# Kernel optimization log

Hardware: AMD Instinct MI355X
Metric: run time of the kernel (lower is better)

The kernel has to match this reference:

```python
import jax, jax.numpy as jnp
import numpy as np

TAIL_BOUND = 3.0
MIN_BIN_WIDTH = 1e-3
MIN_BIN_HEIGHT = 1e-3
SEARCH_EPS = 1e-6


def setup_inputs() -> dict:
    key = jax.random.key(0)
    k1, k2, k3, k4, k5 = jax.random.split(key, 5)
    B, D, K = 8192, 256, 8
    return {
        "x": jax.random.normal(k1, (B, D), dtype=jnp.float32),
        "w_": jax.random.normal(k2, (B, D, K), dtype=jnp.float32),
        "h_": jax.random.normal(k3, (B, D, K), dtype=jnp.float32),
        "dl_": jax.random.normal(k4, (B, D, 1), dtype=jnp.float32),
        "dr_": jax.random.normal(k5, (B, D, 1), dtype=jnp.float32),
    }


def _cumknots(unnorm, min_bin):
    # softmax -> min-width floor -> cumsum with exact 0/1 endpoints
    num_bins = unnorm.shape[-1]
    w = jax.nn.softmax(unnorm, axis=-1)
    w = min_bin + (1.0 - min_bin * num_bins) * w
    cum = jnp.cumsum(w, axis=-1)
    cum = cum.at[..., -1].set(1.0)
    pad = [(0, 0)] * (cum.ndim - 1) + [(1, 0)]
    cum = jnp.pad(cum, pad)
    return w, cum


def reference(x, w_, h_, dl_, dr_):
    num_bins = w_.shape[-1]
    left = bottom = -TAIL_BOUND
    right = top = TAIL_BOUND

    inside = (x >= left) & (x <= right)

    # map to unit interval; clamp keeps masked-out lanes numerically safe
    t = jnp.clip((x - left) / (right - left), 0.0, 1.0)

    widths, cumwidths = _cumknots(w_, MIN_BIN_WIDTH)       # [B,D,K], [B,D,K+1]
    heights, cumheights = _cumknots(h_, MIN_BIN_HEIGHT)

    slopes = heights / widths                              # [B,D,K]
    min1 = jnp.minimum(jnp.abs(slopes[..., :-1]), jnp.abs(slopes[..., 1:]))
    min2 = 0.5 * (widths[..., 1:] * slopes[..., :-1] + widths[..., :-1] * slopes[..., 1:]) \
           / (widths[..., :-1] + widths[..., 1:])
    mins = jnp.minimum(min1, min2)                         # [B,D,K-1]

    d_left = jax.nn.sigmoid(dl_) * 3.0 * slopes[..., :1]
    d_right = jax.nn.sigmoid(dr_) * 3.0 * slopes[..., -1:]
    d_mid = mins * (jnp.sign(slopes[..., :-1]) + jnp.sign(slopes[..., 1:]))
    derivs = jnp.concatenate([d_left, d_mid, d_right], axis=-1)  # [B,D,K+1]

    a = (derivs[..., :-1] + derivs[..., 1:] - 2.0 * slopes) / widths ** 2
    b = (3.0 * slopes - 2.0 * derivs[..., :-1] - derivs[..., 1:]) / widths
    c = derivs[..., :-1]
    d = cumheights[..., :-1]

    # searchsorted: sum(t >= knots) - 1, with eps bump on the last knot
    knots = cumwidths.at[..., -1].add(SEARCH_EPS)
    bin_idx = jnp.sum((t[..., None] >= knots).astype(jnp.int32), axis=-1) - 1
    bin_idx = jnp.clip(bin_idx, 0, num_bins - 1)[..., None]  # [B,D,1]

    take = lambda arr: jnp.take_along_axis(arr, bin_idx, axis=-1)[..., 0]
    ia, ib, ic, id_ = take(a), take(b), take(c), take(d)
    lw = take(cumwidths)

    sx = t - lw
    out_s = ia * sx ** 3 + ib * sx ** 2 + ic * sx + id_
    lad_s = jnp.log(jnp.abs(3.0 * ia * sx ** 2 + 2.0 * ib * sx + ic))

    out_s = jnp.clip(out_s, 0.0, 1.0) * (top - bottom) + bottom
    lad_s = lad_s + jnp.log(top - bottom) - jnp.log(right - left)

    outputs = jnp.where(inside, out_s, x)          # identity tails
    logabsdet = jnp.where(inside, lad_s, 0.0)
    return outputs, logabsdet
```

## Files before the change

### kernel.cpp

```cpp
#include <hip/hip_runtime.h>
#include <math.h>


constexpr int K = 8;
constexpr int E = 4;
constexpr float TAIL = 3.0f;
constexpr float MIN_BIN = 0.001f;
constexpr float SEARCH_EPS = 1e-6f;

typedef float vfloat4 __attribute__((ext_vector_type(4)));

__device__ __forceinline__ float rcpf(float v) {
    return __builtin_amdgcn_rcpf(v);
}

__global__ __launch_bounds__(256) void cbs_kernel(
    const float* __restrict__ x_,
    const float* __restrict__ w_,
    const float* __restrict__ h_,
    const float* __restrict__ dl_,
    const float* __restrict__ dr_,
    float* __restrict__ out,
    float* __restrict__ lad,
    int n)
{
    const int t  = blockIdx.x * blockDim.x + threadIdx.x;
    const int e0 = t * E;
    if (e0 >= n) return;

    const vfloat4* w4 = (const vfloat4*)w_ + 2 * (size_t)e0;
    const vfloat4* h4 = (const vfloat4*)h_ + 2 * (size_t)e0;
    vfloat4 wv[2 * E], hv[2 * E];
    #pragma unroll
    for (int q = 0; q < 2 * E; q++) wv[q] = w4[q];
    #pragma unroll
    for (int q = 0; q < 2 * E; q++) hv[q] = h4[q];
    vfloat4 xv4  = ((const vfloat4*)x_)[t];
    vfloat4 dl4  = ((const vfloat4*)dl_)[t];
    vfloat4 dr4  = ((const vfloat4*)dr_)[t];

    float outs[E], lads[E];

    #pragma unroll
    for (int e = 0; e < E; e++) {
        float wr[K] = {wv[2*e].x, wv[2*e].y, wv[2*e].z, wv[2*e].w,
                       wv[2*e+1].x, wv[2*e+1].y, wv[2*e+1].z, wv[2*e+1].w};
        float hr[K] = {hv[2*e].x, hv[2*e].y, hv[2*e].z, hv[2*e].w,
                       hv[2*e+1].x, hv[2*e+1].y, hv[2*e+1].z, hv[2*e+1].w};
        const float xv = xv4[e], dlv = dl4[e], drv = dr4[e];

        float sw = 0.0f;
        #pragma unroll
        for (int k = 0; k < K; k++) { wr[k] = __expf(wr[k]); sw += wr[k]; }
        float cs = (1.0f - MIN_BIN * K) * rcpf(sw);
        #pragma unroll
        for (int k = 0; k < K; k++) wr[k] = MIN_BIN + cs * wr[k];

        float sh = 0.0f;
        #pragma unroll
        for (int k = 0; k < K; k++) { hr[k] = __expf(hr[k]); sh += hr[k]; }
        float csh = (1.0f - MIN_BIN * K) * rcpf(sh);
        #pragma unroll
        for (int k = 0; k < K; k++) hr[k] = MIN_BIN + csh * hr[k];

        float cw[K + 1]; cw[0] = 0.0f;
        #pragma unroll
        for (int k = 0; k < K; k++) cw[k + 1] = cw[k] + wr[k];
        float ch[K + 1]; ch[0] = 0.0f;
        #pragma unroll
        for (int k = 0; k < K; k++) ch[k + 1] = ch[k] + hr[k];

        float s[K];
        #pragma unroll
        for (int k = 0; k < K; k++) s[k] = hr[k] * rcpf(wr[k]);

        float dv[K + 1];
        dv[0] = rcpf(1.0f + __expf(-dlv)) * 3.0f * s[0];
        dv[K] = rcpf(1.0f + __expf(-drv)) * 3.0f * s[K - 1];
        #pragma unroll
        for (int k = 0; k < K - 1; k++) {
            float two_m1 = 2.0f * fminf(s[k], s[k + 1]);
            float m2x = (wr[k + 1] * s[k] + wr[k] * s[k + 1])
                        * rcpf(wr[k] + wr[k + 1]);
            dv[k + 1] = fminf(two_m1, m2x);
        }

        float tt = (xv + TAIL) * (1.0f / (2.0f * TAIL));
        tt = fminf(fmaxf(tt, 0.0f), 1.0f);

        int bin = 0;
        #pragma unroll
        for (int jj = 1; jj < K; jj++) bin += (tt >= cw[jj]) ? 1 : 0;
        bin += (tt >= 1.0f + SEARCH_EPS) ? 1 : 0;
        if (bin > K - 1) bin = K - 1;

        float wk = wr[0], sk = s[0], d0 = dv[0], d1 = dv[1], lw = cw[0], dd = ch[0];
        #pragma unroll
        for (int k = 1; k < K; k++) {
            bool sel = (bin == k);
            wk = sel ? wr[k]     : wk;
            sk = sel ? s[k]      : sk;
            d0 = sel ? dv[k]     : d0;
            d1 = sel ? dv[k + 1] : d1;
            lw = sel ? cw[k]     : lw;
            dd = sel ? ch[k]     : dd;
        }

        float inv_wk = rcpf(wk);
        float ia = (d0 + d1 - 2.0f * sk) * inv_wk * inv_wk;
        float ib = (3.0f * sk - 2.0f * d0 - d1) * inv_wk;
        float ic = d0;

        float sx = tt - lw;
        float out_s = ((ia * sx + ib) * sx + ic) * sx + dd;
        float der   = (3.0f * ia * sx + 2.0f * ib) * sx + ic;
        float lad_s = __logf(fabsf(der));

        out_s = fminf(fmaxf(out_s, 0.0f), 1.0f) * (2.0f * TAIL) - TAIL;

        bool inside = (xv >= -TAIL) && (xv <= TAIL);
        outs[e] = inside ? out_s : xv;
        lads[e] = inside ? lad_s : 0.0f;
    }

    vfloat4 o4 = {outs[0], outs[1], outs[2], outs[3]};
    vfloat4 l4 = {lads[0], lads[1], lads[2], lads[3]};
    __builtin_nontemporal_store(o4, (vfloat4*)out + t);
    __builtin_nontemporal_store(l4, (vfloat4*)lad + t);
}

extern "C" void kernel_launch(void* const* d_in, const int* in_sizes, int n_in,
                              void* d_out, int out_size, void* d_ws, size_t ws_size,
                              hipStream_t stream) {
    const float* x  = (const float*)d_in[0];
    const float* w  = (const float*)d_in[1];
    const float* h  = (const float*)d_in[2];
    const float* dl = (const float*)d_in[3];
    const float* dr = (const float*)d_in[4];
    int n = in_sizes[0];
    float* out = (float*)d_out;
    float* lad = out + n;

    const int threads = 256;
    const int per_block = threads * E;
    const int blocks = (n + per_block - 1) / per_block;
    cbs_kernel<<<blocks, threads, 0, stream>>>(x, w, h, dl, dr, out, lad, n);
}
```

Baseline: 187.7 us.

## Use block-strided element mapping for coalesced loads and add occupancy hint

Each thread now handles elements spaced 256 apart instead of four contiguous ones. Adjacent lanes therefore read adjacent 32-byte w/h records, which aims to improve memory coalescing. All loads are issued up front behind a sched_barrier, and launch_bounds gains a min-blocks hint to limit register use. In exchange, the x/dl/dr loads and the output stores go from vector to scalar. The bounds check is also removed, so the kernel assumes n is a multiple of 1024.

```diff
diff --git a/kernel.cpp b/kernel.cpp
--- a/kernel.cpp
+++ b/kernel.cpp
@@ -14,7 +14,7 @@
     return __builtin_amdgcn_rcpf(v);
 }
 
-__global__ __launch_bounds__(256) void cbs_kernel(
+__global__ __launch_bounds__(256, 2) void cbs_kernel(
     const float* __restrict__ x_,
     const float* __restrict__ w_,
     const float* __restrict__ h_,
@@ -24,30 +24,33 @@
     float* __restrict__ lad,
     int n)
 {
-    const int t  = blockIdx.x * blockDim.x + threadIdx.x;
-    const int e0 = t * E;
-    if (e0 >= n) return;
+    const int base = blockIdx.x * (256 * E) + threadIdx.x;
 
-    const vfloat4* w4 = (const vfloat4*)w_ + 2 * (size_t)e0;
-    const vfloat4* h4 = (const vfloat4*)h_ + 2 * (size_t)e0;
-    vfloat4 wv[2 * E], hv[2 * E];
+    vfloat4 wv[E][2], hv[E][2];
+    float   xs[E], dls[E], drs[E];
+    int     idx[E];
     #pragma unroll
-    for (int q = 0; q < 2 * E; q++) wv[q] = w4[q];
-    #pragma unroll
-    for (int q = 0; q < 2 * E; q++) hv[q] = h4[q];
-    vfloat4 xv4  = ((const vfloat4*)x_)[t];
-    vfloat4 dl4  = ((const vfloat4*)dl_)[t];
-    vfloat4 dr4  = ((const vfloat4*)dr_)[t];
+    for (int e = 0; e < E; e++) {
+        int i = base + e * 256;
+        idx[e] = i;
+        const vfloat4* w4 = (const vfloat4*)w_ + 2 * (size_t)i;
+        const vfloat4* h4 = (const vfloat4*)h_ + 2 * (size_t)i;
+        wv[e][0] = w4[0]; wv[e][1] = w4[1];
+        hv[e][0] = h4[0]; hv[e][1] = h4[1];
+        xs[e]  = x_[i];
+        dls[e] = dl_[i];
+        drs[e] = dr_[i];
+    }
 
-    float outs[E], lads[E];
+    __builtin_amdgcn_sched_barrier(0);
 
     #pragma unroll
     for (int e = 0; e < E; e++) {
-        float wr[K] = {wv[2*e].x, wv[2*e].y, wv[2*e].z, wv[2*e].w,
-                       wv[2*e+1].x, wv[2*e+1].y, wv[2*e+1].z, wv[2*e+1].w};
-        float hr[K] = {hv[2*e].x, hv[2*e].y, hv[2*e].z, hv[2*e].w,
-                       hv[2*e+1].x, hv[2*e+1].y, hv[2*e+1].z, hv[2*e+1].w};
-        const float xv = xv4[e], dlv = dl4[e], drv = dr4[e];
+        float wr[K] = {wv[e][0].x, wv[e][0].y, wv[e][0].z, wv[e][0].w,
+                       wv[e][1].x, wv[e][1].y, wv[e][1].z, wv[e][1].w};
+        float hr[K] = {hv[e][0].x, hv[e][0].y, hv[e][0].z, hv[e][0].w,
+                       hv[e][1].x, hv[e][1].y, hv[e][1].z, hv[e][1].w};
+        const float xv = xs[e], dlv = dls[e], drv = drs[e];
 
         float sw = 0.0f;
         #pragma unroll
@@ -119,14 +122,9 @@
         out_s = fminf(fmaxf(out_s, 0.0f), 1.0f) * (2.0f * TAIL) - TAIL;
 
         bool inside = (xv >= -TAIL) && (xv <= TAIL);
-        outs[e] = inside ? out_s : xv;
-        lads[e] = inside ? lad_s : 0.0f;
+        __builtin_nontemporal_store(inside ? out_s : xv,   out + idx[e]);
+        __builtin_nontemporal_store(inside ? lad_s : 0.0f, lad + idx[e]);
     }
-
-    vfloat4 o4 = {outs[0], outs[1], outs[2], outs[3]};
-    vfloat4 l4 = {lads[0], lads[1], lads[2], lads[3]};
-    __builtin_nontemporal_store(o4, (vfloat4*)out + t);
-    __builtin_nontemporal_store(l4, (vfloat4*)lad + t);
 }
 
 extern "C" void kernel_launch(void* const* d_in, const int* in_sizes, int n_in,
```

New measurement: 178.9 us. -4.7%, faster.
